# Performance work log

Measured on AMD Instinct MI355X. Metric: run time of the kernel, lower is better.

The kernel has to match this reference:

```python
import jax, jax.numpy as jnp
import numpy as np

EPS = 0.1        # init kwarg eps
MAX_ITER = 100   # init kwarg max_iter
THRESH = 0.1     # hard-coded convergence threshold in forward


def setup_inputs() -> dict:
    key = jax.random.key(0)
    k1, k2 = jax.random.split(key)
    x = jax.random.normal(k1, (8, 2048, 512), dtype=jnp.float32)
    y = jax.random.normal(k2, (8, 2048, 512), dtype=jnp.float32)
    return {"x": x, "y": y}


def _cost_matrix(x, y):
    # cosine distance: 1 - <x_hat, y_hat>
    xn = x / jnp.linalg.norm(x, axis=-1, keepdims=True)
    yn = y / jnp.linalg.norm(y, axis=-1, keepdims=True)
    return 1.0 - jnp.einsum('bnd,bmd->bnm', xn, yn)  # [B, N, M]


def _sinkhorn(C, eps, max_iter):
    B, N, M = C.shape
    mu = jnp.full((B, N), 1.0 / N, dtype=C.dtype)
    nu = jnp.full((B, M), 1.0 / M, dtype=C.dtype)
    log_mu = jnp.log(mu + 1e-8)
    log_nu = jnp.log(nu + 1e-8)

    def Mmat(u, v):
        # (-C + u_i + v_j) / eps
        return (-C + u[:, :, None] + v[:, None, :]) / eps

    def body(carry, _):
        u, v, done = carry
        u_new = eps * (log_mu - jax.nn.logsumexp(Mmat(u, v), axis=-1)) + u
        # torch does logsumexp over dim=-1 of the transpose == axis=-2 here
        v_new = eps * (log_nu - jax.nn.logsumexp(Mmat(u_new, v), axis=-2)) + v
        err = jnp.abs(u_new - u).sum(-1).mean()
        # once converged (err < thresh after an applied update), freeze state
        u_out = jnp.where(done, u, u_new)
        v_out = jnp.where(done, v, v_new)
        done_out = jnp.logical_or(done, err < THRESH)
        return (u_out, v_out, done_out), None

    u0 = jnp.zeros_like(mu)
    v0 = jnp.zeros_like(nu)
    (u, v, _), _ = jax.lax.scan(body, (u0, v0, jnp.array(False)), None, length=max_iter)
    pi = jnp.exp(Mmat(u, v))  # transport plan [B, N, M]
    return pi, mu, nu


def reference(x, y):
    C = _cost_matrix(x, y)
    pi, mu, nu = _sinkhorn(C, EPS, MAX_ITER)
    cost = jnp.sum(pi * C, axis=(-2, -1))  # reduction='none' -> [B]
    return (cost, mu, nu, pi, C)
```

## Files before the change

### kernel.cpp

```cpp
#include <hip/hip_runtime.h>
#include <hip/hip_fp16.h>
#include <hip/hip_cooperative_groups.h>

typedef __attribute__((ext_vector_type(8))) short bf16x8;
typedef __attribute__((ext_vector_type(4))) float f32x4;
typedef __attribute__((ext_vector_type(8))) _Float16 half8;
typedef __attribute__((ext_vector_type(4))) _Float16 half4;


__global__ __launch_bounds__(256) void norm_cast_kernel(
    const float* __restrict__ x, const float* __restrict__ y,
    unsigned short* __restrict__ xnb, unsigned short* __restrict__ ynb,
    float* __restrict__ out, float* __restrict__ us, float* __restrict__ vs,
    float* __restrict__ errb, int* __restrict__ bar)
{
    int tid = blockIdx.x * 256 + threadIdx.x;
    if (tid < 8) out[tid] = 0.0f;
    if (tid < 16384) {
        out[8 + tid]     = 1.0f / 2048.0f;
        out[16392 + tid] = 1.0f / 2048.0f;
        us[tid] = 0.0f;
        vs[tid] = 0.0f;
    }
    if (tid < 128) errb[tid] = 0.0f;
    if (tid < 64)  bar[tid]  = 0;

    int w = tid >> 6;
    int lane = threadIdx.x & 63;
    const float* src = ((w < 16384) ? x : y) + (size_t)(w & 16383) * 512;
    unsigned short* dst = ((w < 16384) ? xnb : ynb) + (size_t)(w & 16383) * 512;

    float4 a = ((const float4*)src)[lane * 2];
    float4 b = ((const float4*)src)[lane * 2 + 1];
    float ss = a.x*a.x + a.y*a.y + a.z*a.z + a.w*a.w
             + b.x*b.x + b.y*b.y + b.z*b.z + b.w*b.w;
#pragma unroll
    for (int off = 32; off > 0; off >>= 1) ss += __shfl_xor(ss, off);
    float rn = rsqrtf(ss);

    float v[8] = {a.x*rn, a.y*rn, a.z*rn, a.w*rn, b.x*rn, b.y*rn, b.z*rn, b.w*rn};
    unsigned short o[8];
#pragma unroll
    for (int i = 0; i < 8; ++i) {
        unsigned int u = __float_as_uint(v[i]);
        o[i] = (unsigned short)((u + 0x7fffu + ((u >> 16) & 1u)) >> 16);
    }
    unsigned int w0 = (unsigned)o[0] | ((unsigned)o[1] << 16);
    unsigned int w1 = (unsigned)o[2] | ((unsigned)o[3] << 16);
    unsigned int w2 = (unsigned)o[4] | ((unsigned)o[5] << 16);
    unsigned int w3 = (unsigned)o[6] | ((unsigned)o[7] << 16);
    uint4 pk; pk.x = w0; pk.y = w1; pk.z = w2; pk.w = w3;
    *(uint4*)(dst + lane * 8) = pk;
}

__global__ __launch_bounds__(256) void gemm_kernel(
    const unsigned short* __restrict__ xnb, const unsigned short* __restrict__ ynb,
    float* __restrict__ Cout, _Float16* __restrict__ G, _Float16* __restrict__ GT)
{
    __shared__ __align__(16) unsigned short smem[128 * 136];
    unsigned short* As = smem;
    unsigned short* Bs = smem + 128 * 64;

    int bid = blockIdx.x;
    int b  = bid >> 8;
    int t  = bid & 255;
    int tn = t >> 4, tm = t & 15;
    const unsigned short* Abase = xnb + ((size_t)b * 2048 + tn * 128) * 512;
    const unsigned short* Bbase = ynb + ((size_t)b * 2048 + tm * 128) * 512;

    int tid = threadIdx.x;
    int wave = tid >> 6, lane = tid & 63;
    int wr = wave >> 1, wc = wave & 1;
    int quad = lane >> 4, l16 = lane & 15;

    f32x4 acc[4][4] = {};

    for (int k0 = 0; k0 < 512; k0 += 64) {
#pragma unroll
        for (int rr = 0; rr < 4; ++rr) {
            int chunk = rr * 256 + tid;
            int row = chunk >> 3;
            int gr  = chunk & 7;
            int sgr = gr ^ (row & 7);
            *(uint4*)(As + row * 64 + sgr * 8) =
                *(const uint4*)(Abase + (size_t)row * 512 + k0 + gr * 8);
            *(uint4*)(Bs + row * 64 + sgr * 8) =
                *(const uint4*)(Bbase + (size_t)row * 512 + k0 + gr * 8);
        }
        __syncthreads();
#pragma unroll
        for (int kk = 0; kk < 64; kk += 32) {
            bf16x8 af[4], bfr[4];
            int g = (kk >> 3) + quad;
#pragma unroll
            for (int i = 0; i < 4; ++i) {
                int rowA = wr * 64 + i * 16 + l16;
                af[i] = *(const bf16x8*)(As + rowA * 64 + ((g ^ (rowA & 7)) << 3));
                int rowB = wc * 64 + i * 16 + l16;
                bfr[i] = *(const bf16x8*)(Bs + rowB * 64 + ((g ^ (rowB & 7)) << 3));
            }
#pragma unroll
            for (int i = 0; i < 4; ++i)
#pragma unroll
                for (int j = 0; j < 4; ++j)
                    acc[i][j] = __builtin_amdgcn_mfma_f32_16x16x32_bf16(
                        af[i], bfr[j], acc[i][j], 0, 0, 0);
        }
        __syncthreads();
    }

    unsigned short* gt = smem;
    size_t cbase = (size_t)b * 2048 * 2048;
#pragma unroll
    for (int i = 0; i < 4; ++i) {
#pragma unroll
        for (int j = 0; j < 4; ++j) {
            int n0l = wr * 64 + i * 16 + quad * 4;
            int ml  = wc * 64 + j * 16 + l16;
            int n0 = tn * 128 + n0l;
            int m  = tm * 128 + ml;
            half4 gv;
#pragma unroll
            for (int rg = 0; rg < 4; ++rg) {
                float c = 1.0f - acc[i][j][rg];
                size_t idx = cbase + (size_t)(n0 + rg) * 2048 + m;
                Cout[idx] = c;
                _Float16 gh = (_Float16)(-10.0f * c);
                G[idx] = gh;
                gv[rg] = gh;
            }
            *(half4*)(gt + ml * 136 + n0l) = gv;
        }
    }
    __syncthreads();
#pragma unroll
    for (int k = 0; k < 8; ++k) {
        int chunk = k * 256 + tid;
        int row = chunk >> 4;
        int c8  = chunk & 15;
        uint4 vv = *(const uint4*)(gt + row * 136 + c8 * 8);
        *(uint4*)((unsigned short*)GT + cbase +
                  (size_t)(tm * 128 + row) * 2048 + tn * 128 + c8 * 8) = vv;
    }
}

__device__ __forceinline__ float row_lse_2048(const _Float16* __restrict__ row,
                                              const float* __restrict__ vec, int lane)
{
    float vals[32];
    float mx = -3.0e38f;
#pragma unroll
    for (int c = 0; c < 4; ++c) {
        int m0 = c * 512 + lane * 8;
        half8 h  = *(const half8*)(row + m0);
        float4 f0 = *(const float4*)(vec + m0);
        float4 f1 = *(const float4*)(vec + m0 + 4);
        float tv[8] = { f0.x + (float)h[0], f0.y + (float)h[1],
                        f0.z + (float)h[2], f0.w + (float)h[3],
                        f1.x + (float)h[4], f1.y + (float)h[5],
                        f1.z + (float)h[6], f1.w + (float)h[7] };
#pragma unroll
        for (int j = 0; j < 8; ++j) { vals[c * 8 + j] = tv[j]; mx = fmaxf(mx, tv[j]); }
    }
#pragma unroll
    for (int off = 32; off > 0; off >>= 1) mx = fmaxf(mx, __shfl_xor(mx, off));
    float s = 0.0f;
#pragma unroll
    for (int i = 0; i < 32; ++i) s += __expf(vals[i] - mx);
#pragma unroll
    for (int off = 32; off > 0; off >>= 1) s += __shfl_xor(s, off);
    return mx + __logf(s);
}

__device__ __forceinline__ void gridbar(int* cnt, int* gen, int nb)
{
    __syncthreads();
    if (threadIdx.x == 0) {
        int g = __hip_atomic_load(gen, __ATOMIC_RELAXED, __HIP_MEMORY_SCOPE_AGENT);
        int v = __hip_atomic_fetch_add(cnt, 1, __ATOMIC_ACQ_REL, __HIP_MEMORY_SCOPE_AGENT);
        if (v == nb - 1) {
            __hip_atomic_store(cnt, 0, __ATOMIC_RELAXED, __HIP_MEMORY_SCOPE_AGENT);
            __hip_atomic_fetch_add(gen, 1, __ATOMIC_RELEASE, __HIP_MEMORY_SCOPE_AGENT);
        } else {
            while (__hip_atomic_load(gen, __ATOMIC_RELAXED, __HIP_MEMORY_SCOPE_AGENT) == g)
                __builtin_amdgcn_s_sleep(1);
            (void)__hip_atomic_load(gen, __ATOMIC_ACQUIRE, __HIP_MEMORY_SCOPE_AGENT);
        }
    }
    __syncthreads();
}

__global__ __launch_bounds__(256, 4) void sinkhorn_kernel(
    const _Float16* __restrict__ G, const _Float16* __restrict__ GT,
    float* __restrict__ us, float* __restrict__ vs, float* __restrict__ errb,
    int* __restrict__ bar)
{
    __shared__ float wred[4];
    int tid = blockIdx.x * 256 + threadIdx.x;
    const float log_mu = logf(1.0f / 2048.0f + 1e-8f);
    int gwave = tid >> 6;
    int wave  = threadIdx.x >> 6;
    int lane  = threadIdx.x & 63;
    const int nwaves = (gridDim.x * 256) >> 6;
    const int nb = (int)gridDim.x;
    int* cnt = bar;
    int* gen = bar + 32;

    for (int it = 0; it < 100; ++it) {
        float werr = 0.0f;
        for (int r = gwave; r < 16384; r += nwaves) {
            int b = r >> 11;
            float lse = row_lse_2048(G + (size_t)r * 2048, vs + (b << 11), lane);
            float un = log_mu - lse;
            werr += fabsf(un - us[r]);
            if (lane == 0) us[r] = un;
        }
        if (lane == 0) wred[wave] = werr;
        __syncthreads();
        if (threadIdx.x == 0)
            atomicAdd(&errb[it], (wred[0] + wred[1] + wred[2] + wred[3]) * 0.1f);
        gridbar(cnt, gen, nb);
        float err = errb[it] * 0.125f;
        for (int r = gwave; r < 16384; r += nwaves) {
            int b = r >> 11;
            float lse = row_lse_2048(GT + (size_t)r * 2048, us + (b << 11), lane);
            if (lane == 0) vs[r] = log_mu - lse;
        }
        gridbar(cnt, gen, nb);
        if (err < 0.1f) break;
    }
}

__global__ __launch_bounds__(256) void pi_cost_kernel(
    const float* __restrict__ C, const float* __restrict__ us, const float* __restrict__ vs,
    float* __restrict__ pi, float* __restrict__ cost)
{
    __shared__ float red[4];
    int r0 = blockIdx.x * 16;
    int b  = r0 >> 11;
    const float* vb = vs + (b << 11);
    int t = threadIdx.x;
    float csum = 0.0f;
#pragma unroll 2
    for (int i = 0; i < 16; ++i) {
        int r = r0 + i;
        const float* Crow = C + (size_t)r * 2048;
        float* Prow = pi + (size_t)r * 2048;
        float u = us[r];
#pragma unroll
        for (int cch = 0; cch < 2; ++cch) {
            int m0 = (cch * 256 + t) * 4;
            float4 cv = *(const float4*)(Crow + m0);
            float4 vv = *(const float4*)(vb + m0);
            float4 p;
            p.x = __expf(u + vv.x - 10.0f * cv.x);
            p.y = __expf(u + vv.y - 10.0f * cv.y);
            p.z = __expf(u + vv.z - 10.0f * cv.z);
            p.w = __expf(u + vv.w - 10.0f * cv.w);
            *(float4*)(Prow + m0) = p;
            csum += p.x * cv.x + p.y * cv.y + p.z * cv.z + p.w * cv.w;
        }
    }
#pragma unroll
    for (int off = 32; off > 0; off >>= 1) csum += __shfl_xor(csum, off);
    int wave = t >> 6, lane = t & 63;
    if (lane == 0) red[wave] = csum;
    __syncthreads();
    if (t == 0) atomicAdd(&cost[b], red[0] + red[1] + red[2] + red[3]);
}

extern "C" void kernel_launch(void* const* d_in, const int* in_sizes, int n_in,
                              void* d_out, int out_size, void* d_ws, size_t ws_size,
                              hipStream_t stream) {
    const float* x = (const float*)d_in[0];
    const float* y = (const float*)d_in[1];
    float* out = (float*)d_out;

    char* w = (char*)d_ws;
    unsigned short* xnb = (unsigned short*)w;
    unsigned short* ynb = (unsigned short*)(w + 16777216);
    float* us   = (float*)(w + 2 * 16777216);
    float* vs   = (float*)(w + 2 * 16777216 + 65536);
    float* errb = (float*)(w + 2 * 16777216 + 2 * 65536);
    int*   bar  = (int*)(w + 2 * 16777216 + 2 * 65536 + 512);

    float* cost = out;
    float* pi   = out + 32776;
    float* Cout = out + 33587208;
    unsigned short* Gh  = (unsigned short*)pi;
    unsigned short* GTh = Gh + 33554432;

    static int coopGrid = 0;
    if (coopGrid == 0) {
        int nb = 0;
        hipError_t e = hipOccupancyMaxActiveBlocksPerMultiprocessor(
            &nb, (const void*)sinkhorn_kernel, 256, 0);
        if (e != hipSuccess || nb < 1) nb = 2;
        int cus = 256;
        hipDeviceProp_t prop;
        if (hipGetDeviceProperties(&prop, 0) == hipSuccess && prop.multiProcessorCount > 0)
            cus = prop.multiProcessorCount;
        long g = (long)nb * cus;
        if (g > 512) g = 512;
        if (g < 64)  g = 64;
        coopGrid = (int)g;
    }

    norm_cast_kernel<<<8192, 256, 0, stream>>>(x, y, xnb, ynb, out, us, vs, errb, bar);
    gemm_kernel<<<2048, 256, 0, stream>>>(xnb, ynb, Cout, (_Float16*)Gh, (_Float16*)GTh);

    const _Float16* Gc  = (const _Float16*)Gh;
    const _Float16* GTc = (const _Float16*)GTh;
    void* cargs[] = { (void*)&Gc, (void*)&GTc, (void*)&us, (void*)&vs,
                      (void*)&errb, (void*)&bar };
    hipLaunchCooperativeKernel((void*)sinkhorn_kernel, dim3(coopGrid), dim3(256),
                               cargs, 0, stream);

    pi_cost_kernel<<<1024, 256, 0, stream>>>(Cout, us, vs, pi, cost);
}
```

Baseline: 600.5 us.

## Use direct global-to-LDS loads in GEMM and split transpose into separate kernel

The GEMM tile loads now use global_load_lds builtins, writing straight into shared memory instead of staging through registers. The XOR swizzle moves from the LDS write side to the global read side. The in-GEMM transpose of G into GT through shared memory is removed, and a separate 64x64 tile transpose kernel builds GT from G afterwards. This shrinks GEMM LDS use and may raise occupancy, but it adds a full extra read and write pass over the fp16 G matrix (8x2048x2048) plus one more kernel launch.

```diff
diff --git a/kernel.cpp b/kernel.cpp
--- a/kernel.cpp
+++ b/kernel.cpp
@@ -6,6 +6,9 @@
 typedef __attribute__((ext_vector_type(4))) float f32x4;
 typedef __attribute__((ext_vector_type(8))) _Float16 half8;
 typedef __attribute__((ext_vector_type(4))) _Float16 half4;
+
+typedef const __attribute__((address_space(1))) void* gas_ptr;
+typedef __attribute__((address_space(3))) void* las_ptr;
 
 
 __global__ __launch_bounds__(256) void norm_cast_kernel(
@@ -55,11 +58,10 @@
 
 __global__ __launch_bounds__(256) void gemm_kernel(
     const unsigned short* __restrict__ xnb, const unsigned short* __restrict__ ynb,
-    float* __restrict__ Cout, _Float16* __restrict__ G, _Float16* __restrict__ GT)
-{
-    __shared__ __align__(16) unsigned short smem[128 * 136];
-    unsigned short* As = smem;
-    unsigned short* Bs = smem + 128 * 64;
+    float* __restrict__ Cout, _Float16* __restrict__ G)
+{
+    __shared__ __align__(16) unsigned short As[128 * 64];
+    __shared__ __align__(16) unsigned short Bs[128 * 64];
 
     int bid = blockIdx.x;
     int b  = bid >> 8;
@@ -77,15 +79,16 @@
 
     for (int k0 = 0; k0 < 512; k0 += 64) {
 #pragma unroll
-        for (int rr = 0; rr < 4; ++rr) {
-            int chunk = rr * 256 + tid;
+        for (int it2 = 0; it2 < 4; ++it2) {
+            int chunk = it2 * 256 + wave * 64 + lane;
             int row = chunk >> 3;
-            int gr  = chunk & 7;
-            int sgr = gr ^ (row & 7);
-            *(uint4*)(As + row * 64 + sgr * 8) =
-                *(const uint4*)(Abase + (size_t)row * 512 + k0 + gr * 8);
-            *(uint4*)(Bs + row * 64 + sgr * 8) =
-                *(const uint4*)(Bbase + (size_t)row * 512 + k0 + gr * 8);
+            int sgr = chunk & 7;
+            int gr  = sgr ^ (row & 7);
+            const unsigned short* sa = Abase + (size_t)row * 512 + k0 + gr * 8;
+            const unsigned short* sb = Bbase + (size_t)row * 512 + k0 + gr * 8;
+            int dst = (it2 * 256 + wave * 64) * 8;
+            __builtin_amdgcn_global_load_lds((gas_ptr)sa, (las_ptr)(As + dst), 16, 0, 0);
+            __builtin_amdgcn_global_load_lds((gas_ptr)sb, (las_ptr)(Bs + dst), 16, 0, 0);
         }
         __syncthreads();
 #pragma unroll
@@ -109,38 +112,51 @@
         __syncthreads();
     }
 
-    unsigned short* gt = smem;
     size_t cbase = (size_t)b * 2048 * 2048;
 #pragma unroll
     for (int i = 0; i < 4; ++i) {
 #pragma unroll
         for (int j = 0; j < 4; ++j) {
-            int n0l = wr * 64 + i * 16 + quad * 4;
-            int ml  = wc * 64 + j * 16 + l16;
-            int n0 = tn * 128 + n0l;
-            int m  = tm * 128 + ml;
-            half4 gv;
+            int n0 = tn * 128 + wr * 64 + i * 16 + quad * 4;
+            int m  = tm * 128 + wc * 64 + j * 16 + l16;
 #pragma unroll
             for (int rg = 0; rg < 4; ++rg) {
                 float c = 1.0f - acc[i][j][rg];
                 size_t idx = cbase + (size_t)(n0 + rg) * 2048 + m;
                 Cout[idx] = c;
-                _Float16 gh = (_Float16)(-10.0f * c);
-                G[idx] = gh;
-                gv[rg] = gh;
+                G[idx] = (_Float16)(-10.0f * c);
             }
-            *(half4*)(gt + ml * 136 + n0l) = gv;
-        }
+        }
+    }
+}
+
+__global__ __launch_bounds__(256) void transpose_kernel(
+    const unsigned short* __restrict__ G, unsigned short* __restrict__ GT)
+{
+    __shared__ __align__(16) unsigned short tile[64][68];
+    int bid = blockIdx.x;
+    int b  = bid >> 10;
+    int t2 = bid & 1023;
+    int tr = t2 >> 5, tc = t2 & 31;
+    int t  = threadIdx.x;
+    int cr = t >> 4;
+    int cc = (t & 15) * 4;
+
+    const unsigned short* src = G + ((size_t)b * 2048 + tr * 64) * 2048 + tc * 64;
+#pragma unroll
+    for (int rr = 0; rr < 4; ++rr) {
+        int row = cr * 4 + rr;
+        *(uint2*)&tile[row][cc] = *(const uint2*)(src + (size_t)row * 2048 + cc);
     }
     __syncthreads();
-#pragma unroll
-    for (int k = 0; k < 8; ++k) {
-        int chunk = k * 256 + tid;
-        int row = chunk >> 4;
-        int c8  = chunk & 15;
-        uint4 vv = *(const uint4*)(gt + row * 136 + c8 * 8);
-        *(uint4*)((unsigned short*)GT + cbase +
-                  (size_t)(tm * 128 + row) * 2048 + tn * 128 + c8 * 8) = vv;
+    unsigned short* dst = GT + ((size_t)b * 2048 + tc * 64) * 2048 + tr * 64;
+#pragma unroll
+    for (int rr = 0; rr < 4; ++rr) {
+        int row = cr * 4 + rr;
+        unsigned int w0 = (unsigned)tile[cc + 0][row] | ((unsigned)tile[cc + 1][row] << 16);
+        unsigned int w1 = (unsigned)tile[cc + 2][row] | ((unsigned)tile[cc + 3][row] << 16);
+        uint2 pk; pk.x = w0; pk.y = w1;
+        *(uint2*)(dst + (size_t)row * 2048 + cc) = pk;
     }
 }
 
@@ -307,7 +323,8 @@
     }
 
     norm_cast_kernel<<<8192, 256, 0, stream>>>(x, y, xnb, ynb, out, us, vs, errb, bar);
-    gemm_kernel<<<2048, 256, 0, stream>>>(xnb, ynb, Cout, (_Float16*)Gh, (_Float16*)GTh);
+    gemm_kernel<<<2048, 256, 0, stream>>>(xnb, ynb, Cout, (_Float16*)Gh);
+    transpose_kernel<<<8192, 256, 0, stream>>>(Gh, GTh);
 
     const _Float16* Gc  = (const _Float16*)Gh;
     const _Float16* GTc = (const _Float16*)GTh;
```

Result: slower. 612.5 us (+2.0%).
